# Kernel tuning notes

Measured on AMD Instinct MI355X. Metric: run time of the kernel, lower is better.

## Reference

```python
import jax, jax.numpy as jnp
import numpy as np


def build_mask_even(kh, kw):
    # Hexnet build_masks: zero one edge column for kernel rows at odd distance
    # from the kernel center (hex neighborhood); returns even-row mask + shift.
    mask = np.ones((kh, kw), dtype=np.float32)
    center = kh // 2
    shift = -1 if center % 2 else 1
    for r in range(kh):
        if abs(center - r) % 2:
            if shift == 1:
                mask[r, -1] = 0.0
            else:
                mask[r, 0] = 0.0
    return mask, shift


def setup_inputs() -> dict:
    key = jax.random.key(0)
    k1, k2, k3 = jax.random.split(key, 3)
    x = jax.random.normal(k1, (16, 128, 128, 128), dtype=jnp.float32)  # NHWC
    kernel = jax.random.normal(k2, (3, 3, 128, 256), dtype=jnp.float32) * 0.05  # HWIO
    bias = jax.random.normal(k3, (256,), dtype=jnp.float32) * 0.05
    return {"x": x, "kernel": kernel, "bias": bias}


def _hconv(x, kernel, bias):
    kh, kw = kernel.shape[0], kernel.shape[1]
    mask_np, shift = build_mask_even(kh, kw)
    kernel_even = kernel * jnp.asarray(mask_np)[:, :, None, None]

    # Odd-row kernel: only the rows at odd distance from center, rolled along width.
    center = kh // 2
    odd_rows = [jnp.roll(kernel_even[r], shift, axis=0)
                for r in range(kh) if abs(center - r) % 2]
    kernel_odd = jnp.stack(odd_rows, axis=0)  # (n_odd, kw, Cin, F)

    dn = ("NHWC", "HWIO", "NHWC")
    strides = (2, 1)  # build() doubles the H stride
    out_even = jax.lax.conv_general_dilated(
        x, kernel_even, window_strides=strides, padding="SAME",
        dimension_numbers=dn)
    out_odd = jax.lax.conv_general_dilated(
        x[:, 1:], kernel_odd, window_strides=strides, padding="SAME",
        dimension_numbers=dn)

    # Interleave rows: even0, odd0, even1, odd1, ... (+ trailing even row if longer)
    he, ho = out_even.shape[1], out_odd.shape[1]
    hm = min(he, ho)
    b, _, w, f = out_even.shape
    out = jnp.stack([out_even[:, :hm], out_odd[:, :hm]], axis=2)
    out = out.reshape(b, 2 * hm, w, f)
    if he > ho:
        out = jnp.concatenate([out, out_even[:, -1:]], axis=1)

    return jax.nn.relu(out + bias)


def reference(x, kernel, bias):
    return _hconv(x, kernel, bias)
```

## Files before the change

kernel.cpp:

```cpp
#include <hip/hip_runtime.h>


#define N_  16
#define H_  128
#define W_  128
#define C_  128
#define F_  256
#define HP  130
#define WP  130

typedef short bf16x8 __attribute__((ext_vector_type(8)));
typedef float f32x4  __attribute__((ext_vector_type(4)));

__device__ __forceinline__ unsigned int bf_bits(float f) {
  unsigned int u = __float_as_uint(f);
  return (u + 0x7FFFu + ((u >> 16) & 1u)) >> 16;
}
__device__ __forceinline__ unsigned int pack2(float a, float b) {
  return bf_bits(a) | (bf_bits(b) << 16);
}

__device__ __forceinline__ void even_tap(int ti, int& dr, int& dc, int& kr, int& kc) {
  switch (ti) {
    case 0:  dr = 0; dc = 0;  kr = 0; kc = 1; break;
    case 1:  dr = 0; dc = 1;  kr = 0; kc = 2; break;
    case 2:  dr = 1; dc = -1; kr = 1; kc = 0; break;
    case 3:  dr = 1; dc = 0;  kr = 1; kc = 1; break;
    case 4:  dr = 1; dc = 1;  kr = 1; kc = 2; break;
    case 5:  dr = 2; dc = 0;  kr = 2; kc = 1; break;
    default: dr = 2; dc = 1;  kr = 2; kc = 2; break;
  }
}

__global__ __launch_bounds__(256) void prep_xpad(
    const float* __restrict__ x, char* __restrict__ xpad) {
  long id = (long)blockIdx.x * 256 + threadIdx.x;
  const long total = (long)N_ * HP * WP * 16;
  if (id >= total) return;
  const int g  = (int)(id & 15);
  long pix = id >> 4;
  const int wp = (int)(pix % WP);
  long t = pix / WP;
  const int hh = (int)(t % HP);
  const int nn = (int)(t / HP);
  const int ww = wp - 1;
  uint4 o = make_uint4(0u, 0u, 0u, 0u);
  if (hh < H_ && ww >= 0 && ww < W_) {
    const float* s = x + (((long)(nn * H_ + hh) * W_ + ww) * C_ + g * 8);
    float4 a = *(const float4*)s;
    float4 b = *(const float4*)(s + 4);
    o.x = pack2(a.x, a.y); o.y = pack2(a.z, a.w);
    o.z = pack2(b.x, b.y); o.w = pack2(b.z, b.w);
  }
  *(uint4*)(xpad + id * 16) = o;
}

__global__ __launch_bounds__(256) void prep_wt3(
    const float* __restrict__ k, char* __restrict__ wt3) {
  int id = blockIdx.x * 256 + threadIdx.x;
  if (id >= 7 * 4 * 256 * 4) return;
  const int j  = id & 3;
  const int f  = (id >> 2) & 255;
  const int cq = (id >> 10) & 3;
  const int ti = id >> 12;
  int dr, dc, kr, kc;
  even_tap(ti, dr, dc, kr, kc);
  const int c0 = cq * 32 + j * 8;
  float v[8];
#pragma unroll
  for (int m = 0; m < 8; ++m)
    v[m] = k[((size_t)(kr * 3 + kc) * C_ + (c0 + m)) * F_ + f];
  uint4 o;
  o.x = pack2(v[0], v[1]); o.y = pack2(v[2], v[3]);
  o.z = pack2(v[4], v[5]); o.w = pack2(v[6], v[7]);
  *(uint4*)(wt3 + (size_t)id * 16) = o;
}

__global__ __launch_bounds__(256, 3) void hconv_mfma(
    const char* __restrict__ xpad,
    const char* __restrict__ wt3,
    const float* __restrict__ bias,
    float* __restrict__ out) {
  __shared__ __align__(16) char smem[49152];

  const int tid = threadIdx.x;
  const int bid = (blockIdx.x & 7) * 512 + (blockIdx.x >> 3);
  const int ft = bid & 1;
  const int h  = (bid >> 1) & 127;
  const int n  = bid >> 8;
  const int p  = h & 1;
  const int nsteps = p ? 16 : 28;

  const int lane = tid & 63;
  const int wid  = tid >> 6;
  const int wr   = wid >> 1;
  const int wc   = wid & 1;
  const int l16  = lane & 15;
  const int lk   = lane >> 4;

  auto step_info = [&](int s, int& dc, int& widx, int& dr) {
    if (p == 0) {
      int ti = s >> 2; widx = ti;
      int kr, kc; even_tap(ti, dr, dc, kr, kc);
    } else {
      int q = s >> 2;
      dr = q >> 1;
      dc = (q & 1) ? 0 : -1;
      widx = (q == 0) ? 0 : (q == 1) ? 1 : (q == 2) ? 5 : 6;
    }
  };

  auto stage = [&](int s, int sel) {
    int dc, widx, dr; step_info(s, dc, widx, dr);
    const int cq = s & 3;
    const char* arow = xpad + ((long)(n * HP + (h + dr)) * WP + (dc + 1)) * 256 + cq * 64;
    const char* brow = wt3 + ((size_t)((widx * 4 + cq) * 256 + ft * 128)) * 64;
    char* dst0 = (char*)smem + sel * 16384;
#pragma unroll
    for (int i = 0; i < 4; ++i) {
      const int L = i * 256 + tid;
      const int r = L >> 3, g = L & 7;
      const int l = g ^ (r & 7);
      const char* srcA = arow + (long)r * 256 + l * 16;
      const char* srcB = brow + r * 64 + (l - 4) * 16;
      const char* src = (l < 4) ? srcA : srcB;
      __builtin_amdgcn_global_load_lds(
          (const __attribute__((address_space(1))) void*)src,
          (__attribute__((address_space(3))) void*)(dst0 + L * 16), 16, 0, 0);
    }
  };

  f32x4 acc[4][4] = {};

  stage(0, 0);
  if (nsteps > 1) stage(1, 1);

  for (int s = 0; s < nsteps; ++s) {
    const int sel = s % 3;
    if (s + 1 < nsteps) {
      asm volatile("s_waitcnt vmcnt(4)" ::: "memory");
    } else {
      asm volatile("s_waitcnt vmcnt(0)" ::: "memory");
    }
    __builtin_amdgcn_s_barrier();
    if (s + 2 < nsteps) stage(s + 2, (s + 2) % 3);

    const char* tb = (const char*)smem + sel * 16384;
    bf16x8 af[4], bfr[4];
#pragma unroll
    for (int m = 0; m < 4; ++m) {
      const int wl = wr * 64 + m * 16 + l16;
      af[m] = *(const bf16x8*)(tb + wl * 128 + ((lk ^ (wl & 7)) * 16));
    }
#pragma unroll
    for (int fi = 0; fi < 4; ++fi) {
      const int fl = wc * 64 + fi * 16 + l16;
      bfr[fi] = *(const bf16x8*)(tb + fl * 128 + (((4 + lk) ^ (fl & 7)) * 16));
    }

    __builtin_amdgcn_s_setprio(1);
#pragma unroll
    for (int m = 0; m < 4; ++m)
#pragma unroll
      for (int fi = 0; fi < 4; ++fi)
        acc[m][fi] = __builtin_amdgcn_mfma_f32_16x16x32_bf16(
            af[m], bfr[fi], acc[m][fi], 0, 0, 0);
    __builtin_amdgcn_s_setprio(0);
  }

#pragma unroll
  for (int fi = 0; fi < 4; ++fi) {
    const int f = ft * 128 + wc * 64 + fi * 16 + l16;
    const float bv = bias[f];
#pragma unroll
    for (int m = 0; m < 4; ++m) {
      const int w = wr * 64 + m * 16 + lk * 4;
      float* o = out + (((size_t)(n * H_ + h) * W_ + w) * F_ + f);
#pragma unroll
      for (int r = 0; r < 4; ++r) {
        float v = acc[m][fi][r] + bv;
        v = v > 0.f ? v : 0.f;
        o[(size_t)r * F_] = v;
      }
    }
  }
}

__device__ __forceinline__ void tap_info11(int t, int& dr, int& dc, int& kr, int& kc) {
  switch (t) {
    case 0:  dr = 0; dc = 0;  kr = 0; kc = 1; break;
    case 1:  dr = 0; dc = 1;  kr = 0; kc = 2; break;
    case 2:  dr = 1; dc = -1; kr = 1; kc = 0; break;
    case 3:  dr = 1; dc = 0;  kr = 1; kc = 1; break;
    case 4:  dr = 1; dc = 1;  kr = 1; kc = 2; break;
    case 5:  dr = 2; dc = 0;  kr = 2; kc = 1; break;
    case 6:  dr = 2; dc = 1;  kr = 2; kc = 2; break;
    case 7:  dr = 0; dc = -1; kr = 0; kc = 1; break;
    case 8:  dr = 0; dc = 0;  kr = 0; kc = 2; break;
    case 9:  dr = 1; dc = -1; kr = 2; kc = 1; break;
    default: dr = 1; dc = 0;  kr = 2; kc = 2; break;
  }
}

__global__ __launch_bounds__(256) void build_w_fb(
    const float* __restrict__ k, unsigned short* __restrict__ wt) {
  int tid = blockIdx.x * 256 + threadIdx.x;
  if (tid >= 11 * F_ * C_) return;
  int c = tid & 127;
  int f = (tid >> 7) & 255;
  int t = tid >> 15;
  int dr, dc, kr, kc;
  tap_info11(t, dr, dc, kr, kc);
  wt[tid] = (unsigned short)bf_bits(k[((kr * 3 + kc) * C_ + c) * F_ + f]);
}

__global__ __launch_bounds__(256, 3) void hconv_fb(
    const float* __restrict__ x,
    const unsigned short* __restrict__ wt,
    const float* __restrict__ bias,
    float* __restrict__ out) {
  __shared__ __align__(16) char smem[49152];
  const int tid = threadIdx.x;
  const int bid = (blockIdx.x & 7) * 1024 + (blockIdx.x >> 3);
  const int ft    = bid & 1;
  const int wtile = (bid >> 1) & 1;
  const int h     = (bid >> 2) & 127;
  const int n     = bid >> 9;
  const int f0 = ft * 128;
  const int w0 = wtile * 64;
  const int p  = h & 1;
  const int tap0   = p ? 7 : 0;
  const int nsteps = p ? 8 : 14;
  const int lane = tid & 63;
  const int wid  = tid >> 6;
  const int l16  = lane & 15;
  const int lk   = lane >> 4;
  const int awl = tid >> 2;
  const int ag2 = tid & 3;
  const int bfl   = tid >> 1;
  const int bhalf = tid & 1;
  float4 ar0, ar1, ar2, ar3;
  uint4  br0, br1, br2, br3;
  auto load_step = [&](int s) {
    const int tap = tap0 + (s >> 1);
    const int cc  = s & 1;
    int dr, dc, kr, kc;
    tap_info11(tap, dr, dc, kr, kc);
    const int hh = h + dr;
    const int wg = w0 + awl + dc;
    const bool av = (hh < H_) && (wg >= 0) && (wg < W_);
    if (av) {
      const float* ap = x + (((long)(n * H_ + hh) * W_ + wg) * C_ + cc * 64 + ag2 * 16);
      ar0 = *(const float4*)(ap);
      ar1 = *(const float4*)(ap + 4);
      ar2 = *(const float4*)(ap + 8);
      ar3 = *(const float4*)(ap + 12);
    } else {
      ar0 = ar1 = ar2 = ar3 = make_float4(0.f, 0.f, 0.f, 0.f);
    }
    const unsigned short* bp =
        wt + ((size_t)(tap * F_ + f0 + bfl) * C_ + cc * 64 + bhalf * 32);
    const uint4* bq = (const uint4*)bp;
    br0 = bq[0]; br1 = bq[1]; br2 = bq[2]; br3 = bq[3];
  };
  auto write_step = [&](int sel) {
    uint4 u0, u1;
    u0.x = pack2(ar0.x, ar0.y); u0.y = pack2(ar0.z, ar0.w);
    u0.z = pack2(ar1.x, ar1.y); u0.w = pack2(ar1.z, ar1.w);
    u1.x = pack2(ar2.x, ar2.y); u1.y = pack2(ar2.z, ar2.w);
    u1.z = pack2(ar3.x, ar3.y); u1.w = pack2(ar3.z, ar3.w);
    char* abase = (char*)smem + sel * 8192 + awl * 128;
    const int sw = awl & 7;
    *(uint4*)(abase + (((2 * ag2)     ^ sw) * 16)) = u0;
    *(uint4*)(abase + (((2 * ag2 + 1) ^ sw) * 16)) = u1;
    char* bbase = (char*)smem + 16384 + sel * 16384 + bfl * 128;
    const int sb = bfl & 7;
    *(uint4*)(bbase + (((bhalf * 4 + 0) ^ sb) * 16)) = br0;
    *(uint4*)(bbase + (((bhalf * 4 + 1) ^ sb) * 16)) = br1;
    *(uint4*)(bbase + (((bhalf * 4 + 2) ^ sb) * 16)) = br2;
    *(uint4*)(bbase + (((bhalf * 4 + 3) ^ sb) * 16)) = br3;
  };
  f32x4 acc[4][2] = {};
  load_step(0);
  write_step(0);
  load_step(1);
  __syncthreads();
  for (int s = 0; s < nsteps; ++s) {
    const int cur = s & 1;
    const char* ab = (const char*)smem + cur * 8192;
    const char* bb = (const char*)smem + 16384 + cur * 16384;
    bf16x8 af[4][2], bfr[2][2];
#pragma unroll
    for (int m = 0; m < 4; ++m)
#pragma unroll
      for (int kkk = 0; kkk < 2; ++kkk) {
        const int wl = m * 16 + l16;
        const int g  = (kkk * 4 + lk) ^ (wl & 7);
        af[m][kkk] = *(const bf16x8*)(ab + wl * 128 + g * 16);
      }
#pragma unroll
    for (int fi = 0; fi < 2; ++fi)
#pragma unroll
      for (int kkk = 0; kkk < 2; ++kkk) {
        const int fl = wid * 32 + fi * 16 + l16;
        const int g  = (kkk * 4 + lk) ^ (fl & 7);
        bfr[fi][kkk] = *(const bf16x8*)(bb + fl * 128 + g * 16);
      }
    if (s + 1 < nsteps) write_step(cur ^ 1);
    if (s + 2 < nsteps) load_step(s + 2);
#pragma unroll
    for (int m = 0; m < 4; ++m)
#pragma unroll
      for (int fi = 0; fi < 2; ++fi)
#pragma unroll
        for (int kkk = 0; kkk < 2; ++kkk)
          acc[m][fi] = __builtin_amdgcn_mfma_f32_16x16x32_bf16(
              af[m][kkk], bfr[fi][kkk], acc[m][fi], 0, 0, 0);
    __syncthreads();
  }
#pragma unroll
  for (int fi = 0; fi < 2; ++fi) {
    const int f = f0 + wid * 32 + fi * 16 + l16;
    const float bv = bias[f];
#pragma unroll
    for (int m = 0; m < 4; ++m) {
      const int w = w0 + m * 16 + lk * 4;
      float* o = out + (((size_t)(n * H_ + h) * W_ + w) * F_ + f);
#pragma unroll
      for (int r = 0; r < 4; ++r) {
        float v = acc[m][fi][r] + bv;
        v = v > 0.f ? v : 0.f;
        o[(size_t)r * F_] = v;
      }
    }
  }
}

extern "C" void kernel_launch(void* const* d_in, const int* in_sizes, int n_in,
                              void* d_out, int out_size, void* d_ws, size_t ws_size,
                              hipStream_t stream) {
  const float* x    = (const float*)d_in[0];
  const float* kern = (const float*)d_in[1];
  const float* bias = (const float*)d_in[2];
  float* out = (float*)d_out;

  const size_t XPAD_BYTES = (size_t)N_ * HP * WP * 256;
  const size_t WT3_BYTES  = (size_t)7 * 4 * 256 * 4 * 16;

  if (ws_size >= XPAD_BYTES + WT3_BYTES) {
    char* xpad = (char*)d_ws;
    char* wt3  = (char*)d_ws + XPAD_BYTES;
    {
      const long total = (long)N_ * HP * WP * 16;
      prep_xpad<<<(int)((total + 255) / 256), 256, 0, stream>>>(x, xpad);
    }
    prep_wt3<<<(7 * 4 * 256 * 4 + 255) / 256, 256, 0, stream>>>(kern, wt3);
    hconv_mfma<<<N_ * H_ * 2, 256, 0, stream>>>(xpad, wt3, bias, out);
  } else {
    unsigned short* wt = (unsigned short*)d_ws;
    build_w_fb<<<(11 * F_ * C_ + 255) / 256, 256, 0, stream>>>(kern, wt);
    hconv_fb<<<N_ * H_ * 2 * 2, 256, 0, stream>>>(x, wt, bias, out);
  }
}
```

Measured before the change: 175.9 us.

## Load MFMA fragments directly from global memory into registers, drop LDS staging

Replaces the LDS triple-buffered global_load_lds pipeline with per-wave direct global loads of A and B fragments into registers, double-buffered across two register sets. This removes LDS traffic and block-wide barriers each step. In exchange, each wave fetches its own operands, so data shared between waves (A across wc, B across wr) is loaded redundantly from global/L2. The loads are also narrower and strided, which lowers coalescing and increases register pressure.

```diff
diff --git a/kernel.cpp b/kernel.cpp
--- a/kernel.cpp
+++ b/kernel.cpp
@@ -81,8 +81,6 @@
     const char* __restrict__ wt3,
     const float* __restrict__ bias,
     float* __restrict__ out) {
-  __shared__ __align__(16) char smem[49152];
-
   const int tid = threadIdx.x;
   const int bid = (blockIdx.x & 7) * 512 + (blockIdx.x >> 3);
   const int ft = bid & 1;
@@ -110,62 +108,41 @@
     }
   };
 
-  auto stage = [&](int s, int sel) {
+  auto loadf = [&](int s, bf16x8* a, bf16x8* b) {
     int dc, widx, dr; step_info(s, dc, widx, dr);
     const int cq = s & 3;
-    const char* arow = xpad + ((long)(n * HP + (h + dr)) * WP + (dc + 1)) * 256 + cq * 64;
-    const char* brow = wt3 + ((size_t)((widx * 4 + cq) * 256 + ft * 128)) * 64;
-    char* dst0 = (char*)smem + sel * 16384;
-#pragma unroll
-    for (int i = 0; i < 4; ++i) {
-      const int L = i * 256 + tid;
-      const int r = L >> 3, g = L & 7;
-      const int l = g ^ (r & 7);
-      const char* srcA = arow + (long)r * 256 + l * 16;
-      const char* srcB = brow + r * 64 + (l - 4) * 16;
-      const char* src = (l < 4) ? srcA : srcB;
-      __builtin_amdgcn_global_load_lds(
-          (const __attribute__((address_space(1))) void*)src,
-          (__attribute__((address_space(3))) void*)(dst0 + L * 16), 16, 0, 0);
-    }
+    const char* arow = xpad +
+        ((long)(n * HP + (h + dr)) * WP + (dc + 1) + wr * 64) * 256 + cq * 64 + lk * 16;
+    const char* brow = wt3 +
+        (size_t)(((widx * 4 + cq) * 256) + ft * 128 + wc * 64 + l16) * 64 + lk * 16;
+#pragma unroll
+    for (int m = 0; m < 4; ++m)
+      a[m] = *(const bf16x8*)(arow + (m * 16 + l16) * 256);
+#pragma unroll
+    for (int fi = 0; fi < 4; ++fi)
+      b[fi] = *(const bf16x8*)(brow + fi * 16 * 64);
   };
 
   f32x4 acc[4][4] = {};
 
-  stage(0, 0);
-  if (nsteps > 1) stage(1, 1);
-
-  for (int s = 0; s < nsteps; ++s) {
-    const int sel = s % 3;
-    if (s + 1 < nsteps) {
-      asm volatile("s_waitcnt vmcnt(4)" ::: "memory");
-    } else {
-      asm volatile("s_waitcnt vmcnt(0)" ::: "memory");
-    }
-    __builtin_amdgcn_s_barrier();
-    if (s + 2 < nsteps) stage(s + 2, (s + 2) % 3);
-
-    const char* tb = (const char*)smem + sel * 16384;
-    bf16x8 af[4], bfr[4];
-#pragma unroll
-    for (int m = 0; m < 4; ++m) {
-      const int wl = wr * 64 + m * 16 + l16;
-      af[m] = *(const bf16x8*)(tb + wl * 128 + ((lk ^ (wl & 7)) * 16));
-    }
-#pragma unroll
-    for (int fi = 0; fi < 4; ++fi) {
-      const int fl = wc * 64 + fi * 16 + l16;
-      bfr[fi] = *(const bf16x8*)(tb + fl * 128 + (((4 + lk) ^ (fl & 7)) * 16));
-    }
-
-    __builtin_amdgcn_s_setprio(1);
+  auto mstep = [&](bf16x8* a, bf16x8* b) {
 #pragma unroll
     for (int m = 0; m < 4; ++m)
 #pragma unroll
       for (int fi = 0; fi < 4; ++fi)
         acc[m][fi] = __builtin_amdgcn_mfma_f32_16x16x32_bf16(
-            af[m], bfr[fi], acc[m][fi], 0, 0, 0);
-    __builtin_amdgcn_s_setprio(0);
+            a[m], b[fi], acc[m][fi], 0, 0, 0);
+  };
+
+  bf16x8 a0[4], b0[4], a1[4], b1[4];
+  loadf(0, a0, b0);
+  loadf(1, a1, b1);
+
+  for (int s = 0; s < nsteps; s += 2) {
+    mstep(a0, b0);
+    if (s + 2 < nsteps) loadf(s + 2, a0, b0);
+    mstep(a1, b1);
+    if (s + 3 < nsteps) loadf(s + 3, a1, b1);
   }
 
 #pragma unroll
```

Result: slower. 345.9 us (+96.7%).
